# Optimization experiments

Measured on AMD Instinct MI355X. Metric: run time of the kernel, lower is better.

Reference implementation:

```python
import jax, jax.numpy as jnp
import numpy as np

N, IN_C, HEADS, OUT_C = 4096, 256, 4, 64
NEG_SLOPE = 0.2


def setup_inputs() -> dict:
    key = jax.random.key(0)
    k1, k2, k3, k4, k5 = jax.random.split(key, 5)
    x = jax.random.normal(k1, (N, IN_C), dtype=jnp.float32)
    adj = jax.random.randint(k2, (N, N), 0, 2, dtype=jnp.int32)
    # xavier-uniform style scales
    s_w = float(np.sqrt(6.0 / (IN_C + HEADS * OUT_C)))
    s_a = float(np.sqrt(6.0 / (HEADS + OUT_C)))
    W = jax.random.uniform(k3, (IN_C, HEADS * OUT_C), jnp.float32, -s_w, s_w)
    att_l = jax.random.uniform(k4, (HEADS, OUT_C), jnp.float32, -s_a, s_a)
    att_r = jax.random.uniform(k5, (HEADS, OUT_C), jnp.float32, -s_a, s_a)
    bias = jnp.zeros((HEADS * OUT_C,), jnp.float32)
    return {"x": x, "adj": adj, "W": W, "att_l": att_l, "att_r": att_r, "bias": bias}


def reference(x, adj, W, att_l, att_r, bias):
    n = x.shape[0]
    h = (x @ W).reshape(n, HEADS, OUT_C)              # [N, H, C]
    el = jnp.einsum('nhc,hc->nh', h, att_l)           # [N, H]
    er = jnp.einsum('nhc,hc->nh', h, att_r)           # [N, H]
    e = el[:, None, :] + er[None, :, :]               # [N, N, H]
    e = jnp.where(e >= 0, e, NEG_SLOPE * e)           # leaky_relu
    mask = (adj > 0)[:, :, None]                      # [N, N, 1]
    e = jnp.where(mask, e, -jnp.inf)
    alpha = jax.nn.softmax(e, axis=1)                 # softmax over j
    out = jnp.einsum('ijh,jhc->ihc', alpha, h)        # [N, H, C]
    out = out.reshape(n, HEADS * OUT_C) + bias
    return out
```

## Files before the change

### kernel.cpp

```cpp
#include <hip/hip_runtime.h>
#include <hip/hip_bf16.h>
#include <stdint.h>

typedef float f32x4 __attribute__((ext_vector_type(4)));
typedef short s16x8 __attribute__((ext_vector_type(8)));
typedef int   i32x4 __attribute__((ext_vector_type(4)));
typedef _Float16 f16x4 __attribute__((ext_vector_type(4)));
typedef unsigned int u32;

#define NNODES 4096
#define INC    256
#define OUTF   256
#define NEG    0.2f
#define SJ     8
#define JL     512

__device__ __forceinline__ unsigned short f2bf(float f) {
  unsigned u = __float_as_uint(f);
  u += 0x7FFFu + ((u >> 16) & 1u);
  return (unsigned short)(u >> 16);
}
__device__ __forceinline__ unsigned encf(float x) {
  unsigned u = __float_as_uint(x);
  return (u & 0x80000000u) ? ~u : (u | 0x80000000u);
}
__device__ __forceinline__ float decf(unsigned e) {
  unsigned u = (e & 0x80000000u) ? (e ^ 0x80000000u) : ~e;
  return __uint_as_float(u);
}

__global__ __launch_bounds__(256) void k_feat(
    const float* __restrict__ x, const float* __restrict__ W,
    const float* __restrict__ attl, const float* __restrict__ attr,
    unsigned short* __restrict__ hT, float* __restrict__ el_t,
    u32* __restrict__ QS, unsigned* __restrict__ M_enc)
{
  __shared__ float smbuf[33024];
  float* xs  = smbuf;
  float* wsl = smbuf + 16640;
  const int tid  = threadIdx.x;
  const int lane = tid & 63, wid = tid >> 6;
  const int hb = blockIdx.x, nb = blockIdx.y;
  const int n0 = nb * 64, c0 = hb * 64;
  const int ty = tid >> 4, tx = tid & 15;

#pragma unroll
  for (int q = 0; q < 16; ++q) {
    const int n = wid * 16 + q;
    __builtin_amdgcn_global_load_lds(x + (size_t)(n0 + n) * INC + lane * 4,
                                     xs + n * 260, 16, 0, 0);
  }
#pragma unroll
  for (int q = 0; q < 16; ++q) {
    const int kb = (wid * 16 + q) * 4;
    __builtin_amdgcn_global_load_lds(
        W + (size_t)(kb + (lane >> 4)) * OUTF + c0 + (lane & 15) * 4,
        wsl + kb * 64, 16, 0, 0);
  }
  __syncthreads();

  f32x4 acc[4];
#pragma unroll
  for (int r = 0; r < 4; ++r) acc[r] = (f32x4){0.f, 0.f, 0.f, 0.f};

#pragma unroll 4
  for (int k4 = 0; k4 < 64; ++k4) {
    f32x4 a[4], b[4];
#pragma unroll
    for (int r = 0; r < 4; ++r)
      a[r] = *(const f32x4*)(xs + (ty * 4 + r) * 260 + k4 * 4);
#pragma unroll
    for (int kk = 0; kk < 4; ++kk)
      b[kk] = *(const f32x4*)(wsl + (k4 * 4 + kk) * 64 + tx * 4);
#pragma unroll
    for (int r = 0; r < 4; ++r)
#pragma unroll
      for (int kk = 0; kk < 4; ++kk)
        acc[r] += a[r][kk] * b[kk];
  }

  f32x4 al = *(const f32x4*)(attl + c0 + tx * 4);
  f32x4 ar = *(const f32x4*)(attr + c0 + tx * 4);
  float pl[4], pr[4];
#pragma unroll
  for (int r = 0; r < 4; ++r) {
    pl[r] = acc[r][0] * al[0] + acc[r][1] * al[1] + acc[r][2] * al[2] + acc[r][3] * al[3];
    pr[r] = acc[r][0] * ar[0] + acc[r][1] * ar[1] + acc[r][2] * ar[2] + acc[r][3] * ar[3];
  }
#pragma unroll
  for (int m = 1; m < 16; m <<= 1) {
#pragma unroll
    for (int r = 0; r < 4; ++r) {
      pl[r] += __shfl_xor(pl[r], m, 64);
      pr[r] += __shfl_xor(pr[r], m, 64);
    }
  }
  if (tx == 0) {
#pragma unroll
    for (int r = 0; r < 4; ++r) {
      el_t[hb * NNODES + n0 + ty * 4 + r] = pl[r];
      float q = __expf(pr[r]);
      float s = __expf(NEG * pr[r]);
      QS[hb * NNODES + n0 + ty * 4 + r] = (u32)f2bf(q) | ((u32)f2bf(s) << 16);
    }
  }
  float mx = fmaxf(fmaxf(pr[0], pr[1]), fmaxf(pr[2], pr[3]));
  mx = fmaxf(mx, __shfl_xor(mx, 16, 64));
  mx = fmaxf(mx, __shfl_xor(mx, 32, 64));
  if (lane == 0) atomicMax(M_enc + hb, encf(mx));

  __syncthreads();
  float* smT = smbuf;
#pragma unroll
  for (int r = 0; r < 4; ++r)
#pragma unroll
    for (int j = 0; j < 4; ++j)
      smT[(tx * 4 + j) * 65 + ty * 4 + r] = acc[r][j];
  __syncthreads();
  {
    const int c = tid >> 2, g0 = tid & 3;
    const int key = c & 7;
#pragma unroll
    for (int t = 0; t < 2; ++t) {
      const int gg = g0 + t * 4;
      unsigned v[4];
#pragma unroll
      for (int i = 0; i < 4; ++i) {
        unsigned lo = f2bf(smT[c * 65 + gg * 8 + 2 * i]);
        unsigned hi = f2bf(smT[c * 65 + gg * 8 + 2 * i + 1]);
        v[i] = lo | (hi << 16);
      }
      unsigned short* dst = hT + (size_t)(c0 + c) * NNODES + n0 + ((gg ^ key) * 8);
      *(uint4*)dst = make_uint4(v[0], v[1], v[2], v[3]);
    }
  }
}

__global__ __launch_bounds__(512, 2) void k_gat(
    const int* __restrict__ adj, const unsigned short* __restrict__ hT,
    const float* __restrict__ el_t, const u32* __restrict__ QS,
    const unsigned* __restrict__ M_enc,
    _Float16* __restrict__ nump, float* __restrict__ denp)
{
  __shared__ __align__(16) unsigned short hbuf[256 * 256];
  __shared__ __align__(16) u32 qsb[4 * JL];

  const int tid = threadIdx.x;
  const int wid = tid >> 6, lane = tid & 63;
  const int l15 = lane & 15, lg = lane >> 4;
  const int i0 = blockIdx.x * 128 + wid * 16;
  const int js = blockIdx.y;
  const int j0 = js * JL;
  const int key = l15 & 7;

  float P[4], R[4];
#pragma unroll
  for (int h = 0; h < 4; ++h) {
    float el  = el_t[h * NNODES + i0 + l15];
    float M   = decf(M_enc[h]);
    float sE  = el + M;
    float mih = fmaxf(sE, NEG * sE);
    P[h] = __expf(el - mih);
    R[h] = __expf(NEG * el - mih);
  }

  __builtin_amdgcn_global_load_lds(
      QS + (size_t)(wid >> 1) * NNODES + j0 + (wid & 1) * 256 + lane * 4,
      qsb + (wid >> 1) * JL + (wid & 1) * 256, 16, 0, 0);

  const int* asrc = adj + (size_t)(i0 + l15) * NNODES + j0 + lg * 8;

  f32x4 acc[4][4];
  f32x4 accd[4];
#pragma unroll
  for (int h = 0; h < 4; ++h) {
    accd[h] = (f32x4){0.f, 0.f, 0.f, 0.f};
#pragma unroll
    for (int c = 0; c < 4; ++c) acc[h][c] = (f32x4){0.f, 0.f, 0.f, 0.f};
  }
  s16x8 ones;
#pragma unroll
  for (int e = 0; e < 8; ++e) ones[e] = (short)0x3F80;

#define STAGE(p)                                                                 \
  do {                                                                           \
    _Pragma("unroll")                                                            \
    for (int q = 0; q < 16; ++q) {                                               \
      const int c2 = wid * 32 + q * 2;                                           \
      __builtin_amdgcn_global_load_lds(                                          \
          hT + (size_t)(c2 + (lane >> 5)) * NNODES + j0 + (p) * 256 + (lane & 31) * 8, \
          hbuf + c2 * 256, 16, 0, 0);                                            \
    }                                                                            \
  } while (0)

  STAGE(0);

#pragma unroll
  for (int p = 0; p < 2; ++p) {
    if (p == 1) {
      __syncthreads();
      STAGE(1);
    }
    i32x4 a0 = *(const i32x4*)(asrc + p * 256);
    i32x4 a1 = *(const i32x4*)(asrc + p * 256 + 4);
    __syncthreads();

#pragma unroll
    for (int K = 0; K < 8; ++K) {
      const int nK = (K < 7) ? (K + 1) : 7;
      i32x4 na0 = *(const i32x4*)(asrc + p * 256 + nK * 32);
      i32x4 na1 = *(const i32x4*)(asrc + p * 256 + nK * 32 + 4);

      const int pos = (K >> 1) * 64 + ((((K & 1) * 4 + lg) ^ key) * 8);

#pragma unroll
      for (int h = 0; h < 4; ++h) {
        const unsigned short* lb = hbuf + (h * 64 + l15) * 256 + pos;
        s16x8 b0 = *(const s16x8*)(lb);
        s16x8 b1 = *(const s16x8*)(lb + 16 * 256);
        s16x8 b2 = *(const s16x8*)(lb + 32 * 256);
        s16x8 b3 = *(const s16x8*)(lb + 48 * 256);
        const u32* qrow = qsb + h * JL + p * 256 + K * 32 + lg * 8;
        i32x4 q0 = *(const i32x4*)(qrow);
        i32x4 q1 = *(const i32x4*)(qrow + 4);

        float w[8];
#pragma unroll
        for (int e = 0; e < 4; ++e) {
          u32 m0 = (a0[e] > 0) ? (u32)q0[e] : 0u;
          u32 m1 = (a1[e] > 0) ? (u32)q1[e] : 0u;
          float qq0 = __uint_as_float(m0 << 16);
          float ss0 = __uint_as_float(m0 & 0xffff0000u);
          float qq1 = __uint_as_float(m1 << 16);
          float ss1 = __uint_as_float(m1 & 0xffff0000u);
          w[e]     = fmaxf(P[h] * qq0, R[h] * ss0);
          w[e + 4] = fmaxf(P[h] * qq1, R[h] * ss1);
        }
        union { u32 uu[4]; s16x8 v; } af;
#pragma unroll
        for (int pp = 0; pp < 4; ++pp)
          asm("v_cvt_pk_bf16_f32 %0, %1, %2"
              : "=v"(af.uu[pp]) : "v"(w[2 * pp]), "v"(w[2 * pp + 1]));

        acc[h][0] = __builtin_amdgcn_mfma_f32_16x16x32_bf16(af.v, b0,   acc[h][0], 0, 0, 0);
        acc[h][1] = __builtin_amdgcn_mfma_f32_16x16x32_bf16(af.v, b1,   acc[h][1], 0, 0, 0);
        acc[h][2] = __builtin_amdgcn_mfma_f32_16x16x32_bf16(af.v, b2,   acc[h][2], 0, 0, 0);
        acc[h][3] = __builtin_amdgcn_mfma_f32_16x16x32_bf16(af.v, b3,   acc[h][3], 0, 0, 0);
        accd[h]   = __builtin_amdgcn_mfma_f32_16x16x32_bf16(af.v, ones, accd[h],   0, 0, 0);
      }
      a0 = na0; a1 = na1;
    }
  }
#undef STAGE

  const int orow = i0 + lg * 4;
#pragma unroll
  for (int h = 0; h < 4; ++h) {
    _Float16* np = nump + ((size_t)js * NNODES + orow) * OUTF + h * 64 + l15;
#pragma unroll
    for (int c = 0; c < 4; ++c)
#pragma unroll
      for (int r = 0; r < 4; ++r)
        np[r * OUTF + c * 16] = (_Float16)acc[h][c][r];
  }
  if (l15 == 0) {
    float* dp = denp + ((size_t)js * NNODES + orow) * 4;
#pragma unroll
    for (int h = 0; h < 4; ++h)
#pragma unroll
      for (int r = 0; r < 4; ++r) dp[r * 4 + h] = accd[h][r];
  }
}

__global__ __launch_bounds__(256) void k_div(
    const _Float16* __restrict__ nump, const float* __restrict__ denp,
    const float* __restrict__ bias, float* __restrict__ out)
{
  const int q  = blockIdx.x * 256 + threadIdx.x;
  const int n  = q >> 6;
  const int c4 = (q & 63) * 4;
  const int h  = c4 >> 6;
  f32x4 s = {0.f, 0.f, 0.f, 0.f};
  float d = 0.f;
#pragma unroll
  for (int t = 0; t < SJ; ++t) {
    f16x4 v = *(const f16x4*)(nump + ((size_t)t * NNODES + n) * OUTF + c4);
    s[0] += (float)v[0]; s[1] += (float)v[1];
    s[2] += (float)v[2]; s[3] += (float)v[3];
    d += denp[((size_t)t * NNODES + n) * 4 + h];
  }
  f32x4 b = *(const f32x4*)(bias + c4);
  float r = __builtin_amdgcn_rcpf(d);
  f32x4 o = s * r + b;
  *(f32x4*)(out + (size_t)n * OUTF + c4) = o;
}

extern "C" void kernel_launch(void* const* d_in, const int* in_sizes, int n_in,
                              void* d_out, int out_size, void* d_ws, size_t ws_size,
                              hipStream_t stream)
{
  const float* x    = (const float*)d_in[0];
  const int*   adj  = (const int*)d_in[1];
  const float* W    = (const float*)d_in[2];
  const float* attl = (const float*)d_in[3];
  const float* attr = (const float*)d_in[4];
  const float* bias = (const float*)d_in[5];
  float* out = (float*)d_out;
  char*  ws  = (char*)d_ws;

  unsigned short* hT  = (unsigned short*)ws;
  float*     el_t  = (float*)(ws + (2u << 20));
  u32*       QS    = (u32*)(ws + (2u << 20) + (64u << 10));
  unsigned*  M_enc = (unsigned*)(ws + (2u << 20) + (128u << 10));
  float*     denp  = (float*)(ws + (2u << 20) + (192u << 10));
  _Float16*  nump  = (_Float16*)(ws + (3u << 20));

  hipMemsetAsync(M_enc, 0, 16, stream);
  k_feat<<<dim3(4, 64), 256, 0, stream>>>(x, W, attl, attr, hT, el_t, QS, M_enc);
  k_gat<<<dim3(32, SJ), 512, 0, stream>>>(adj, hT, el_t, QS, M_enc, nump, denp);
  k_div<<<dim3(1024), 256, 0, stream>>>(nump, denp, bias, out);
}
```

Measured before the change: 68.58 us.

## Split GAT heads across warps with 1024-thread blocks of 64 rows

Each warp in k_gat now handles a single head for 16 rows, instead of all four heads. Blocks become 1024 threads covering 64 rows, and the grid doubles. This cuts per-warp accumulator registers by four times and raises wave parallelism. The cost is that the adj tile is reloaded by four warps per row group, and each block stages the same 128KB of hT in LDS for half as many rows, which doubles LDS staging traffic per output. The launch_bounds value of 1024,4 is unrealistic given the LDS usage, so occupancy is likely limited to one block per CU.

After: 79.22 us. +15.5%, slower.

```diff
diff --git a/kernel.cpp b/kernel.cpp
--- a/kernel.cpp
+++ b/kernel.cpp
@@ -136,7 +136,7 @@
   }
 }
 
-__global__ __launch_bounds__(512, 2) void k_gat(
+__global__ __launch_bounds__(1024, 4) void k_gat(
     const int* __restrict__ adj, const unsigned short* __restrict__ hT,
     const float* __restrict__ el_t, const u32* __restrict__ QS,
     const unsigned* __restrict__ M_enc,
@@ -148,36 +148,32 @@
   const int tid = threadIdx.x;
   const int wid = tid >> 6, lane = tid & 63;
   const int l15 = lane & 15, lg = lane >> 4;
-  const int i0 = blockIdx.x * 128 + wid * 16;
+  const int h  = wid & 3;
+  const int ic = wid >> 2;
+  const int i0 = blockIdx.x * 64;
   const int js = blockIdx.y;
   const int j0 = js * JL;
+  const int irow = i0 + ic * 16 + l15;
   const int key = l15 & 7;
 
-  float P[4], R[4];
-#pragma unroll
-  for (int h = 0; h < 4; ++h) {
-    float el  = el_t[h * NNODES + i0 + l15];
-    float M   = decf(M_enc[h]);
-    float sE  = el + M;
-    float mih = fmaxf(sE, NEG * sE);
-    P[h] = __expf(el - mih);
-    R[h] = __expf(NEG * el - mih);
-  }
-
-  __builtin_amdgcn_global_load_lds(
-      QS + (size_t)(wid >> 1) * NNODES + j0 + (wid & 1) * 256 + lane * 4,
-      qsb + (wid >> 1) * JL + (wid & 1) * 256, 16, 0, 0);
-
-  const int* asrc = adj + (size_t)(i0 + l15) * NNODES + j0 + lg * 8;
-
-  f32x4 acc[4][4];
-  f32x4 accd[4];
-#pragma unroll
-  for (int h = 0; h < 4; ++h) {
-    accd[h] = (f32x4){0.f, 0.f, 0.f, 0.f};
-#pragma unroll
-    for (int c = 0; c < 4; ++c) acc[h][c] = (f32x4){0.f, 0.f, 0.f, 0.f};
-  }
+  const float el = el_t[h * NNODES + irow];
+  const float M  = decf(M_enc[h]);
+  const float sE = el + M;
+  const float mih = fmaxf(sE, NEG * sE);
+  const float P = __expf(el - mih);
+  const float R = __expf(NEG * el - mih);
+
+  if (wid < 8)
+    __builtin_amdgcn_global_load_lds(
+        QS + (size_t)(wid >> 1) * NNODES + j0 + (wid & 1) * 256 + lane * 4,
+        qsb + (wid >> 1) * JL + (wid & 1) * 256, 16, 0, 0);
+
+  const int* asrc = adj + (size_t)irow * NNODES + j0 + lg * 8;
+
+  f32x4 acc[4];
+  f32x4 accd = (f32x4){0.f, 0.f, 0.f, 0.f};
+#pragma unroll
+  for (int c = 0; c < 4; ++c) acc[c] = (f32x4){0.f, 0.f, 0.f, 0.f};
   s16x8 ones;
 #pragma unroll
   for (int e = 0; e < 8; ++e) ones[e] = (short)0x3F80;
@@ -185,8 +181,8 @@
 #define STAGE(p)                                                                 \
   do {                                                                           \
     _Pragma("unroll")                                                            \
-    for (int q = 0; q < 16; ++q) {                                               \
-      const int c2 = wid * 32 + q * 2;                                           \
+    for (int q = 0; q < 8; ++q) {                                                \
+      const int c2 = wid * 16 + q * 2;                                           \
       __builtin_amdgcn_global_load_lds(                                          \
           hT + (size_t)(c2 + (lane >> 5)) * NNODES + j0 + (p) * 256 + (lane & 31) * 8, \
           hbuf + c2 * 256, 16, 0, 0);                                            \
@@ -212,63 +208,56 @@
       i32x4 na1 = *(const i32x4*)(asrc + p * 256 + nK * 32 + 4);
 
       const int pos = (K >> 1) * 64 + ((((K & 1) * 4 + lg) ^ key) * 8);
-
-#pragma unroll
-      for (int h = 0; h < 4; ++h) {
-        const unsigned short* lb = hbuf + (h * 64 + l15) * 256 + pos;
-        s16x8 b0 = *(const s16x8*)(lb);
-        s16x8 b1 = *(const s16x8*)(lb + 16 * 256);
-        s16x8 b2 = *(const s16x8*)(lb + 32 * 256);
-        s16x8 b3 = *(const s16x8*)(lb + 48 * 256);
-        const u32* qrow = qsb + h * JL + p * 256 + K * 32 + lg * 8;
-        i32x4 q0 = *(const i32x4*)(qrow);
-        i32x4 q1 = *(const i32x4*)(qrow + 4);
-
-        float w[8];
-#pragma unroll
-        for (int e = 0; e < 4; ++e) {
-          u32 m0 = (a0[e] > 0) ? (u32)q0[e] : 0u;
-          u32 m1 = (a1[e] > 0) ? (u32)q1[e] : 0u;
-          float qq0 = __uint_as_float(m0 << 16);
-          float ss0 = __uint_as_float(m0 & 0xffff0000u);
-          float qq1 = __uint_as_float(m1 << 16);
-          float ss1 = __uint_as_float(m1 & 0xffff0000u);
-          w[e]     = fmaxf(P[h] * qq0, R[h] * ss0);
-          w[e + 4] = fmaxf(P[h] * qq1, R[h] * ss1);
-        }
-        union { u32 uu[4]; s16x8 v; } af;
-#pragma unroll
-        for (int pp = 0; pp < 4; ++pp)
-          asm("v_cvt_pk_bf16_f32 %0, %1, %2"
-              : "=v"(af.uu[pp]) : "v"(w[2 * pp]), "v"(w[2 * pp + 1]));
-
-        acc[h][0] = __builtin_amdgcn_mfma_f32_16x16x32_bf16(af.v, b0,   acc[h][0], 0, 0, 0);
-        acc[h][1] = __builtin_amdgcn_mfma_f32_16x16x32_bf16(af.v, b1,   acc[h][1], 0, 0, 0);
-        acc[h][2] = __builtin_amdgcn_mfma_f32_16x16x32_bf16(af.v, b2,   acc[h][2], 0, 0, 0);
-        acc[h][3] = __builtin_amdgcn_mfma_f32_16x16x32_bf16(af.v, b3,   acc[h][3], 0, 0, 0);
-        accd[h]   = __builtin_amdgcn_mfma_f32_16x16x32_bf16(af.v, ones, accd[h],   0, 0, 0);
+      const unsigned short* lb = hbuf + (h * 64 + l15) * 256 + pos;
+      s16x8 b0 = *(const s16x8*)(lb);
+      s16x8 b1 = *(const s16x8*)(lb + 16 * 256);
+      s16x8 b2 = *(const s16x8*)(lb + 32 * 256);
+      s16x8 b3 = *(const s16x8*)(lb + 48 * 256);
+      const u32* qrow = qsb + h * JL + p * 256 + K * 32 + lg * 8;
+      i32x4 q0 = *(const i32x4*)(qrow);
+      i32x4 q1 = *(const i32x4*)(qrow + 4);
+
+      float w[8];
+#pragma unroll
+      for (int e = 0; e < 4; ++e) {
+        u32 m0 = (a0[e] > 0) ? (u32)q0[e] : 0u;
+        u32 m1 = (a1[e] > 0) ? (u32)q1[e] : 0u;
+        float qq0 = __uint_as_float(m0 << 16);
+        float ss0 = __uint_as_float(m0 & 0xffff0000u);
+        float qq1 = __uint_as_float(m1 << 16);
+        float ss1 = __uint_as_float(m1 & 0xffff0000u);
+        w[e]     = fmaxf(P * qq0, R * ss0);
+        w[e + 4] = fmaxf(P * qq1, R * ss1);
       }
+      union { u32 uu[4]; s16x8 v; } af;
+#pragma unroll
+      for (int pp = 0; pp < 4; ++pp)
+        asm("v_cvt_pk_bf16_f32 %0, %1, %2"
+            : "=v"(af.uu[pp]) : "v"(w[2 * pp]), "v"(w[2 * pp + 1]));
+
+      acc[0] = __builtin_amdgcn_mfma_f32_16x16x32_bf16(af.v, b0,   acc[0], 0, 0, 0);
+      acc[1] = __builtin_amdgcn_mfma_f32_16x16x32_bf16(af.v, b1,   acc[1], 0, 0, 0);
+      acc[2] = __builtin_amdgcn_mfma_f32_16x16x32_bf16(af.v, b2,   acc[2], 0, 0, 0);
+      acc[3] = __builtin_amdgcn_mfma_f32_16x16x32_bf16(af.v, b3,   acc[3], 0, 0, 0);
+      accd   = __builtin_amdgcn_mfma_f32_16x16x32_bf16(af.v, ones, accd,   0, 0, 0);
+
       a0 = na0; a1 = na1;
     }
   }
 #undef STAGE
 
-  const int orow = i0 + lg * 4;
-#pragma unroll
-  for (int h = 0; h < 4; ++h) {
-    _Float16* np = nump + ((size_t)js * NNODES + orow) * OUTF + h * 64 + l15;
-#pragma unroll
-    for (int c = 0; c < 4; ++c)
-#pragma unroll
-      for (int r = 0; r < 4; ++r)
-        np[r * OUTF + c * 16] = (_Float16)acc[h][c][r];
-  }
+  const int orow = i0 + ic * 16 + lg * 4;
+  _Float16* np = nump + ((size_t)js * NNODES + orow) * OUTF + h * 64 + l15;
+#pragma unroll
+  for (int c = 0; c < 4; ++c)
+#pragma unroll
+    for (int r = 0; r < 4; ++r)
+      np[r * OUTF + c * 16] = (_Float16)acc[c][r];
+
   if (l15 == 0) {
-    float* dp = denp + ((size_t)js * NNODES + orow) * 4;
-#pragma unroll
-    for (int h = 0; h < 4; ++h)
-#pragma unroll
-      for (int r = 0; r < 4; ++r) dp[r * 4 + h] = accd[h][r];
+    float* dp = denp + ((size_t)js * NNODES + orow) * 4 + h;
+#pragma unroll
+    for (int r = 0; r < 4; ++r) dp[r * 4] = accd[r];
   }
 }
 
@@ -317,6 +306,6 @@
 
   hipMemsetAsync(M_enc, 0, 16, stream);
   k_feat<<<dim3(4, 64), 256, 0, stream>>>(x, W, attl, attr, hT, el_t, QS, M_enc);
-  k_gat<<<dim3(32, SJ), 512, 0, stream>>>(adj, hT, el_t, QS, M_enc, nump, denp);
+  k_gat<<<dim3(64, SJ), 1024, 0, stream>>>(adj, hT, el_t, QS, M_enc, nump, denp);
   k_div<<<dim3(1024), 256, 0, stream>>>(nump, denp, bias, out);
 }
```

## Split feature stage into prep, attention-logit, and bf16 MFMA projection kernels

Applied to the files above, without the earlier changes.

Replaces the single fp32 FMA feature kernel with three kernels. The first precomputes W·att_l/att_r and a bf16 swizzled transpose of W. The second computes el/er directly from x using the folded weights and converts x to bf16. The third does the projection h = xW with bf16 MFMA instructions. This moves the dense projection onto matrix cores and removes the reduction over h for the attention logits. The cost is two extra launches, extra workspace traffic for xbf and WT, and reduced precision in the projection and in the logits, which are now taken from x·(W·att) rather than from h.

New measurement: 62.49 us. 8.9% less time.

```diff
diff --git a/kernel.cpp b/kernel.cpp
--- a/kernel.cpp
+++ b/kernel.cpp
@@ -9,11 +9,10 @@
 typedef unsigned int u32;
 
 #define NNODES 4096
-#define INC    256
-#define OUTF   256
 #define NEG    0.2f
 #define SJ     8
 #define JL     512
+#define OUTF   256
 
 __device__ __forceinline__ unsigned short f2bf(float f) {
   unsigned u = __float_as_uint(f);
@@ -29,111 +28,175 @@
   return __uint_as_float(u);
 }
 
-__global__ __launch_bounds__(256) void k_feat(
-    const float* __restrict__ x, const float* __restrict__ W,
-    const float* __restrict__ attl, const float* __restrict__ attr,
-    unsigned short* __restrict__ hT, float* __restrict__ el_t,
-    u32* __restrict__ QS, unsigned* __restrict__ M_enc)
-{
-  __shared__ float smbuf[33024];
-  float* xs  = smbuf;
-  float* wsl = smbuf + 16640;
-  const int tid  = threadIdx.x;
-  const int lane = tid & 63, wid = tid >> 6;
-  const int hb = blockIdx.x, nb = blockIdx.y;
-  const int n0 = nb * 64, c0 = hb * 64;
-  const int ty = tid >> 4, tx = tid & 15;
-
+__global__ __launch_bounds__(256) void k_prep(
+    const float* __restrict__ W, const float* __restrict__ attl,
+    const float* __restrict__ attr,
+    unsigned short* __restrict__ WT, float* __restrict__ Wlr)
+{
+  __shared__ float wt[8 * 256];
+  __shared__ float att_s[512];
+  const int tid = threadIdx.x;
+  const int kr = tid >> 5, l32 = tid & 31;
+  const int k = blockIdx.x * 8 + kr;
+  const float* wrow = W + (size_t)k * 256 + l32 * 8;
+  f32x4 w0 = *(const f32x4*)(wrow);
+  f32x4 w1 = *(const f32x4*)(wrow + 4);
+  *(f32x4*)(wt + kr * 256 + l32 * 8)     = w0;
+  *(f32x4*)(wt + kr * 256 + l32 * 8 + 4) = w1;
+  att_s[tid]       = attl[tid];
+  att_s[256 + tid] = attr[tid];
+  __syncthreads();
+
+  float pl = 0.f, pr = 0.f;
+#pragma unroll
+  for (int i = 0; i < 4; ++i) {
+    pl += w0[i] * att_s[l32 * 8 + i] + w1[i] * att_s[l32 * 8 + 4 + i];
+    pr += w0[i] * att_s[256 + l32 * 8 + i] + w1[i] * att_s[256 + l32 * 8 + 4 + i];
+  }
+  pl += __shfl_xor(pl, 1, 64); pl += __shfl_xor(pl, 2, 64); pl += __shfl_xor(pl, 4, 64);
+  pr += __shfl_xor(pr, 1, 64); pr += __shfl_xor(pr, 2, 64); pr += __shfl_xor(pr, 4, 64);
+  if ((l32 & 7) == 0) {
+    Wlr[k * 8 + (l32 >> 3)]     = pl;
+    Wlr[k * 8 + 4 + (l32 >> 3)] = pr;
+  }
+  {
+    const int c = tid;
+    unsigned v[4];
+#pragma unroll
+    for (int i = 0; i < 4; ++i) {
+      unsigned lo = f2bf(wt[(2 * i) * 256 + c]);
+      unsigned hi = f2bf(wt[(2 * i + 1) * 256 + c]);
+      v[i] = lo | (hi << 16);
+    }
+    const int gW = blockIdx.x;
+    const int pos = (gW & 24) | ((gW & 7) ^ (c & 7));
+    *(uint4*)(WT + (size_t)c * 256 + pos * 8) = make_uint4(v[0], v[1], v[2], v[3]);
+  }
+}
+
+__global__ __launch_bounds__(256) void k_el(
+    const float* __restrict__ x, const float* __restrict__ Wlr,
+    float* __restrict__ el_t, u32* __restrict__ QS,
+    unsigned* __restrict__ M_enc, unsigned short* __restrict__ xbf)
+{
+  __shared__ float wls[16 * 145];
+  __shared__ float er_s[64];
+  const int tid = threadIdx.x;
+  {
+    f32x4 a = *(const f32x4*)(Wlr + tid * 8);
+    f32x4 b = *(const f32x4*)(Wlr + tid * 8 + 4);
+    float* d = wls + (tid >> 4) * 145 + (tid & 15) * 9;
+    *(f32x4*)d = a; *(f32x4*)(d + 4) = b;
+  }
+  __syncthreads();
+  const int nl = tid >> 4, l15 = tid & 15;
+  const int n = blockIdx.x * 16 + nl;
+  f32x4 xv[4];
+#pragma unroll
+  for (int i = 0; i < 4; ++i)
+    xv[i] = *(const f32x4*)(x + (size_t)n * 256 + l15 * 16 + i * 4);
+  f32x4 al = {0.f,0.f,0.f,0.f}, ar = {0.f,0.f,0.f,0.f};
+  const float* wb = wls + l15 * 145;
+#pragma unroll
+  for (int i = 0; i < 16; ++i) {
+    float xi = xv[i >> 2][i & 3];
+    f32x4 wl = *(const f32x4*)(wb + i * 9);
+    f32x4 wr = *(const f32x4*)(wb + i * 9 + 4);
+    al += xi * wl; ar += xi * wr;
+  }
+#pragma unroll
+  for (int m = 1; m < 16; m <<= 1)
+#pragma unroll
+    for (int c = 0; c < 4; ++c) {
+      al[c] += __shfl_xor(al[c], m, 64);
+      ar[c] += __shfl_xor(ar[c], m, 64);
+    }
+  if (l15 == 0) {
+#pragma unroll
+    for (int h = 0; h < 4; ++h) {
+      el_t[h * NNODES + n] = al[h];
+      float q = __expf(ar[h]);
+      float s = __expf(NEG * ar[h]);
+      QS[h * NNODES + n] = (u32)f2bf(q) | ((u32)f2bf(s) << 16);
+      er_s[nl * 4 + h] = ar[h];
+    }
+  }
+  {
+    u32 pk[8];
+#pragma unroll
+    for (int i = 0; i < 8; ++i) {
+      unsigned lo = f2bf(xv[(2 * i) >> 2][(2 * i) & 3]);
+      unsigned hi = f2bf(xv[(2 * i + 1) >> 2][(2 * i + 1) & 3]);
+      pk[i] = lo | (hi << 16);
+    }
+    const int key = n & 7;
+    const int g0 = l15 * 2;
+    const int p0 = (g0 & 24) | ((g0 & 7) ^ key);
+    const int p1 = (g0 & 24) | (((g0 + 1) & 7) ^ key);
+    unsigned short* xb = xbf + (size_t)n * 256;
+    *(uint4*)(xb + p0 * 8) = make_uint4(pk[0], pk[1], pk[2], pk[3]);
+    *(uint4*)(xb + p1 * 8) = make_uint4(pk[4], pk[5], pk[6], pk[7]);
+  }
+  __syncthreads();
+  if (tid < 64) {
+    float v = er_s[tid];
+    v = fmaxf(v, __shfl_xor(v, 4, 64));
+    v = fmaxf(v, __shfl_xor(v, 8, 64));
+    v = fmaxf(v, __shfl_xor(v, 16, 64));
+    v = fmaxf(v, __shfl_xor(v, 32, 64));
+    if (tid < 4) atomicMax(M_enc + tid, encf(v));
+  }
+}
+
+__global__ __launch_bounds__(256) void k_hmm(
+    const unsigned short* __restrict__ xbf, const unsigned short* __restrict__ WT,
+    unsigned short* __restrict__ hT)
+{
+  __shared__ __align__(16) unsigned short xs[128 * 256];
+  __shared__ __align__(16) unsigned short ws[64 * 256];
+  const int tid = threadIdx.x, wv = tid >> 6, lane = tid & 63;
+  const int l15 = lane & 15, lg = lane >> 4;
+  const int c0 = blockIdx.x * 64, n0 = blockIdx.y * 128;
 #pragma unroll
   for (int q = 0; q < 16; ++q) {
-    const int n = wid * 16 + q;
-    __builtin_amdgcn_global_load_lds(x + (size_t)(n0 + n) * INC + lane * 4,
-                                     xs + n * 260, 16, 0, 0);
-  }
-#pragma unroll
-  for (int q = 0; q < 16; ++q) {
-    const int kb = (wid * 16 + q) * 4;
+    const int r2 = (wv * 16 + q) * 2;
     __builtin_amdgcn_global_load_lds(
-        W + (size_t)(kb + (lane >> 4)) * OUTF + c0 + (lane & 15) * 4,
-        wsl + kb * 64, 16, 0, 0);
+        xbf + (size_t)(n0 + r2 + (lane >> 5)) * 256 + (lane & 31) * 8,
+        xs + r2 * 256, 16, 0, 0);
+  }
+#pragma unroll
+  for (int q = 0; q < 8; ++q) {
+    const int r2 = (wv * 8 + q) * 2;
+    __builtin_amdgcn_global_load_lds(
+        WT + (size_t)(c0 + r2 + (lane >> 5)) * 256 + (lane & 31) * 8,
+        ws + r2 * 256, 16, 0, 0);
   }
   __syncthreads();
-
-  f32x4 acc[4];
-#pragma unroll
-  for (int r = 0; r < 4; ++r) acc[r] = (f32x4){0.f, 0.f, 0.f, 0.f};
-
-#pragma unroll 4
-  for (int k4 = 0; k4 < 64; ++k4) {
-    f32x4 a[4], b[4];
-#pragma unroll
-    for (int r = 0; r < 4; ++r)
-      a[r] = *(const f32x4*)(xs + (ty * 4 + r) * 260 + k4 * 4);
-#pragma unroll
-    for (int kk = 0; kk < 4; ++kk)
-      b[kk] = *(const f32x4*)(wsl + (k4 * 4 + kk) * 64 + tx * 4);
-#pragma unroll
-    for (int r = 0; r < 4; ++r)
-#pragma unroll
-      for (int kk = 0; kk < 4; ++kk)
-        acc[r] += a[r][kk] * b[kk];
-  }
-
-  f32x4 al = *(const f32x4*)(attl + c0 + tx * 4);
-  f32x4 ar = *(const f32x4*)(attr + c0 + tx * 4);
-  float pl[4], pr[4];
-#pragma unroll
-  for (int r = 0; r < 4; ++r) {
-    pl[r] = acc[r][0] * al[0] + acc[r][1] * al[1] + acc[r][2] * al[2] + acc[r][3] * al[3];
-    pr[r] = acc[r][0] * ar[0] + acc[r][1] * ar[1] + acc[r][2] * ar[2] + acc[r][3] * ar[3];
-  }
-#pragma unroll
-  for (int m = 1; m < 16; m <<= 1) {
+  f32x4 acc[8];
+#pragma unroll
+  for (int nt = 0; nt < 8; ++nt) acc[nt] = (f32x4){0.f,0.f,0.f,0.f};
+  const int key = l15 & 7;
+#pragma unroll
+  for (int kk = 0; kk < 8; ++kk) {
+    const int G = kk * 4 + lg;
+    const int pos = (G & 24) | ((G & 7) ^ key);
+    s16x8 a = *(const s16x8*)(ws + (wv * 16 + l15) * 256 + pos * 8);
+#pragma unroll
+    for (int nt = 0; nt < 8; ++nt) {
+      s16x8 b = *(const s16x8*)(xs + (nt * 16 + l15) * 256 + pos * 8);
+      acc[nt] = __builtin_amdgcn_mfma_f32_16x16x32_bf16(a, b, acc[nt], 0, 0, 0);
+    }
+  }
+#pragma unroll
+  for (int nt = 0; nt < 8; ++nt)
 #pragma unroll
     for (int r = 0; r < 4; ++r) {
-      pl[r] += __shfl_xor(pl[r], m, 64);
-      pr[r] += __shfl_xor(pr[r], m, 64);
-    }
-  }
-  if (tx == 0) {
-#pragma unroll
-    for (int r = 0; r < 4; ++r) {
-      el_t[hb * NNODES + n0 + ty * 4 + r] = pl[r];
-      float q = __expf(pr[r]);
-      float s = __expf(NEG * pr[r]);
-      QS[hb * NNODES + n0 + ty * 4 + r] = (u32)f2bf(q) | ((u32)f2bf(s) << 16);
-    }
-  }
-  float mx = fmaxf(fmaxf(pr[0], pr[1]), fmaxf(pr[2], pr[3]));
-  mx = fmaxf(mx, __shfl_xor(mx, 16, 64));
-  mx = fmaxf(mx, __shfl_xor(mx, 32, 64));
-  if (lane == 0) atomicMax(M_enc + hb, encf(mx));
-
-  __syncthreads();
-  float* smT = smbuf;
-#pragma unroll
-  for (int r = 0; r < 4; ++r)
-#pragma unroll
-    for (int j = 0; j < 4; ++j)
-      smT[(tx * 4 + j) * 65 + ty * 4 + r] = acc[r][j];
-  __syncthreads();
-  {
-    const int c = tid >> 2, g0 = tid & 3;
-    const int key = c & 7;
-#pragma unroll
-    for (int t = 0; t < 2; ++t) {
-      const int gg = g0 + t * 4;
-      unsigned v[4];
-#pragma unroll
-      for (int i = 0; i < 4; ++i) {
-        unsigned lo = f2bf(smT[c * 65 + gg * 8 + 2 * i]);
-        unsigned hi = f2bf(smT[c * 65 + gg * 8 + 2 * i + 1]);
-        v[i] = lo | (hi << 16);
-      }
-      unsigned short* dst = hT + (size_t)(c0 + c) * NNODES + n0 + ((gg ^ key) * 8);
-      *(uint4*)dst = make_uint4(v[0], v[1], v[2], v[3]);
-    }
-  }
+      const int c = c0 + wv * 16 + lg * 4 + r;
+      const int nloc = nt * 16 + l15;
+      const int gl = nloc >> 3;
+      const int posn = (gl & 8) | ((gl & 7) ^ (c & 7));
+      hT[(size_t)c * NNODES + n0 + posn * 8 + (nloc & 7)] = f2bf(acc[nt][r]);
+    }
 }
 
 __global__ __launch_bounds__(512, 2) void k_gat(
@@ -308,15 +371,20 @@
   float* out = (float*)d_out;
   char*  ws  = (char*)d_ws;
 
-  unsigned short* hT  = (unsigned short*)ws;
+  unsigned short* hT   = (unsigned short*)ws;
   float*     el_t  = (float*)(ws + (2u << 20));
   u32*       QS    = (u32*)(ws + (2u << 20) + (64u << 10));
   unsigned*  M_enc = (unsigned*)(ws + (2u << 20) + (128u << 10));
   float*     denp  = (float*)(ws + (2u << 20) + (192u << 10));
+  unsigned short* WT = (unsigned short*)(ws + (2u << 20) + (704u << 10));
+  float*     Wlr   = (float*)(ws + (2u << 20) + (832u << 10));
   _Float16*  nump  = (_Float16*)(ws + (3u << 20));
+  unsigned short* xbf = (unsigned short*)(ws + (17u << 20));
 
   hipMemsetAsync(M_enc, 0, 16, stream);
-  k_feat<<<dim3(4, 64), 256, 0, stream>>>(x, W, attl, attr, hT, el_t, QS, M_enc);
+  k_prep<<<32, 256, 0, stream>>>(W, attl, attr, WT, Wlr);
+  k_el<<<256, 256, 0, stream>>>(x, Wlr, el_t, QS, M_enc, xbf);
+  k_hmm<<<dim3(4, 32), 256, 0, stream>>>(xbf, WT, hT);
   k_gat<<<dim3(32, SJ), 512, 0, stream>>>(adj, hT, el_t, QS, M_enc, nump, denp);
-  k_div<<<dim3(1024), 256, 0, stream>>>(nump, denp, bias, out);
-}
+  k_div<<<1024, 256, 0, stream>>>(nump, denp, bias, out);
+}
```
